# Performance work log

Measured on AMD Instinct MI355X. Metric: run time of the kernel, lower is better.

Reference implementation:

```python
import jax, jax.numpy as jnp
import numpy as np
from jax import lax

BOS, EOS = 1, 2
MAX_LEN = 16
BEAM = 4
VOCAB = 32000
INF = 1e9


def _gather_beams(x, idx):
    # x: [B, K, ...] or [B, K]; idx: [B, k]
    if x.ndim == 3:
        return jnp.take_along_axis(x, idx[:, :, None], axis=1)
    return jnp.take_along_axis(x, idx, axis=1)


def setup_inputs() -> dict:
    key = jax.random.key(0)
    k1, k2, k3, k4 = jax.random.split(key, 4)
    B, S, D = 16, 128, 512
    return {
        "src_input": jax.random.randint(k1, (B, S), 0, VOCAB),
        "E_src": jax.random.normal(k2, (VOCAB, D), jnp.float32) * 0.02,
        "E_tgt": jax.random.normal(k3, (VOCAB, D), jnp.float32) * 0.02,
        "W": jax.random.normal(k4, (D, VOCAB), jnp.float32) * 0.02,
        "b": jnp.zeros((VOCAB,), jnp.float32),
    }


def _beam_search(src_input, E_src, E_tgt, W, b):
    B = src_input.shape[0]
    # tile_by_beam: repeat each batch row beam_size times
    src = jnp.repeat(src_input, BEAM, axis=0)                     # [B*BEAM, S]
    # stub encoder: embedding + masked mean pool (pad token = 0)
    enc = E_src[src]                                              # [B*BEAM, S, D]
    keep = (src != 0).astype(enc.dtype)[..., None]
    pooled = (enc * keep).sum(1) / jnp.maximum(keep.sum(1), 1.0)  # [B*BEAM, D]

    alive_seq = jnp.zeros((B, BEAM, MAX_LEN), jnp.int32).at[:, :, 0].set(BOS)
    alive_lp = jnp.full((B, BEAM), -jnp.inf, jnp.float32).at[:, 0].set(0.0)
    fin_seq = jnp.zeros((B, BEAM, MAX_LEN), jnp.int32)
    fin_scores = jnp.full((B, BEAM), -INF, jnp.float32)
    fin_flags = jnp.zeros((B, BEAM), bool)
    batch_fin = jnp.zeros((B,), bool)
    batch_idx = jnp.arange(B)[:, None]

    for t in range(MAX_LEN - 1):
        # stub decoder: last-token embedding + encoder summary -> vocab logits
        last = alive_seq[:, :, t].reshape(B * BEAM)
        logits = (E_tgt[last] + pooled) @ W + b                   # [B*BEAM, V]
        lp = jax.nn.log_softmax(logits, axis=-1).reshape(B, BEAM, VOCAB)
        log_probs = alive_lp[:, :, None] + lp                     # [B, BEAM, V]
        lpen = jnp.float32(t + 1)
        flat = (log_probs / lpen).reshape(B, BEAM * VOCAB)
        topk_scores, topk_ids = lax.top_k(flat, BEAM * 2)         # [B, 2*BEAM]
        topk_lp = topk_scores * lpen
        if t == 0:
            beam_idx = jnp.tile(jnp.arange(BEAM), (B, 2))
        else:
            beam_idx = topk_ids // VOCAB
        tok = topk_ids % VOCAB
        topk_seq = alive_seq[batch_idx, beam_idx]                 # [B, 2*BEAM, L]
        topk_seq = topk_seq.at[:, :, t + 1].set(tok.astype(jnp.int32))
        topk_fin = tok == EOS
        # alive set: penalize finished candidates
        curr = topk_scores + topk_fin.astype(jnp.float32) * -INF
        _, a_idx = lax.top_k(curr, BEAM)
        alive_seq = _gather_beams(topk_seq, a_idx)
        alive_lp = _gather_beams(topk_lp, a_idx)
        # finished set: penalize unfinished + already-finished batches
        fs = (topk_scores + (1.0 - topk_fin.astype(jnp.float32)) * -INF
              + batch_fin[:, None].astype(jnp.float32) * -INF)
        cand_seq = jnp.concatenate([fin_seq, topk_seq], axis=1)   # [B, 3*BEAM, L]
        cand_sc = jnp.concatenate([fin_scores, fs], axis=1)
        cand_fl = jnp.concatenate([fin_flags, topk_fin], axis=1)
        _, f_idx = lax.top_k(cand_sc, BEAM)
        fin_seq = _gather_beams(cand_seq, f_idx)
        fin_scores = _gather_beams(cand_sc, f_idx)
        fin_flags = _gather_beams(cand_fl, f_idx)
        # batch-finished lower-bound test
        lb_alive = alive_lp[:, 0] / lpen
        lowest_fin = jnp.min(fin_scores * fin_flags.astype(jnp.float32), axis=1)
        lowest_fin = lowest_fin + (1.0 - jnp.all(fin_flags, axis=1).astype(jnp.float32)) * -INF
        batch_fin = batch_fin | (lowest_fin >= lb_alive)
    return fin_seq, fin_scores


def reference(src_input, E_src, E_tgt, W, b):
    fin_seq, _ = _beam_search(src_input, E_src, E_tgt, W, b)
    return fin_seq[:, 0]  # one_best_output [B, MAX_LEN] int32
```

## Files before the change

### kernel.cpp

```cpp
#include <hip/hip_runtime.h>
#include <math.h>

#define BATCH 16
#define SRCLEN 128
#define DIM 512
#define VOCABSZ 32000
#define BEAM 4
#define MAXLEN 16
#define NROWS (BATCH*BEAM)
#define BOS_TOK 1
#define EOS_TOK 2
#define NEGINF 1e9f
#define CHUNKS 8
#define CHUNK 4000
#define PCH 8
#define PCL (SRCLEN/PCH)

__device__ inline unsigned long long packkey(float v, int idx) {
    unsigned int fb = __float_as_uint(v);
    fb = fb ^ ((fb >> 31) ? 0xFFFFFFFFu : 0x80000000u);
    return ((unsigned long long)fb << 32) | (unsigned long long)(0xFFFFFFFFu - (unsigned int)idx);
}
__device__ inline float unpack_val(unsigned long long k) {
    unsigned int fb = (unsigned int)(k >> 32);
    fb = fb ^ ((fb >> 31) ? 0x80000000u : 0xFFFFFFFFu);
    return __uint_as_float(fb);
}
__device__ inline int unpack_id(unsigned long long k) {
    return (int)(0xFFFFFFFFu - (unsigned int)(k & 0xFFFFFFFFu));
}
__device__ inline unsigned long long shflxor64(unsigned long long x, int mask) {
    unsigned int lo = (unsigned int)x, hi = (unsigned int)(x >> 32);
    lo = (unsigned int)__shfl_xor((int)lo, mask, 64);
    hi = (unsigned int)__shfl_xor((int)hi, mask, 64);
    return ((unsigned long long)hi << 32) | (unsigned long long)lo;
}
__device__ inline unsigned long long wavemax64(unsigned long long k) {
#pragma unroll
    for (int off = 1; off < 64; off <<= 1) {
        unsigned long long o = shflxor64(k, off);
        k = (o > k) ? o : k;
    }
    return k;
}

__global__ __launch_bounds__(512) void k_pool2(const int* __restrict__ src,
                                               const float* __restrict__ Esrc,
                                               float* __restrict__ pp, float* __restrict__ pcnt) {
    int b = blockIdx.x, c = blockIdx.y;
    int d = threadIdx.x;
    float acc = 0.f, cnt = 0.f;
#pragma unroll
    for (int s = 0; s < PCL; ++s) {
        int tok = src[b * SRCLEN + c * PCL + s];
        if (tok != 0) { acc += Esrc[(size_t)tok * DIM + d]; cnt += 1.f; }
    }
    pp[(b * PCH + c) * DIM + d] = acc;
    if (d == 0) pcnt[b * PCH + c] = cnt;
}

__global__ __launch_bounds__(512) void k_poolred(const float* __restrict__ pp,
                                                 const float* __restrict__ pcnt,
                                                 float* __restrict__ pooled) {
    int b = blockIdx.x;
    int d = threadIdx.x;
    float acc = 0.f, cnt = 0.f;
#pragma unroll
    for (int c = 0; c < PCH; ++c) { acc += pp[(b * PCH + c) * DIM + d]; cnt += pcnt[b * PCH + c]; }
    pooled[b * DIM + d] = acc / fmaxf(cnt, 1.f);
}

__global__ __launch_bounds__(1024) void k_init(int* __restrict__ alive_seq, float* __restrict__ alive_lp,
                                               int* __restrict__ fin_seq, float* __restrict__ fin_scores,
                                               int* __restrict__ fin_flags, int* __restrict__ batch_fin) {
    int tid = threadIdx.x;
    alive_seq[tid] = (tid % MAXLEN == 0) ? BOS_TOK : 0;
    fin_seq[tid] = 0;
    if (tid < NROWS) {
        alive_lp[tid] = (tid % BEAM == 0) ? 0.f : -INFINITY;
        fin_scores[tid] = -NEGINF;
        fin_flags[tid] = 0;
    }
    if (tid < BATCH) batch_fin[tid] = 0;
}

__global__ __launch_bounds__(512) void k_x(const float* __restrict__ Etgt,
                                           const float* __restrict__ pooled,
                                           const int* __restrict__ alive_seq, int t,
                                           float* __restrict__ xT) {
    int i = blockIdx.x;
    int d = threadIdx.x;
    int last = alive_seq[i * MAXLEN + t];
    float v = Etgt[(size_t)last * DIM + d] + pooled[(i >> 2) * DIM + d];
    xT[d * NROWS + i] = v;
}

template<int GDLEN>
__global__ __launch_bounds__(256) void k_gemm8(const float* __restrict__ xT,
                                               const float* __restrict__ W,
                                               float* __restrict__ partial) {
    int lane = threadIdx.x & 63;
    int r0 = __builtin_amdgcn_readfirstlane((threadIdx.x >> 6) * 16);
    int v0 = blockIdx.x * 256 + lane * 4;
    int z  = blockIdx.z;
    int d0 = z * GDLEN;

    float4 acc[16];
#pragma unroll
    for (int i = 0; i < 16; ++i) acc[i] = make_float4(0.f, 0.f, 0.f, 0.f);

    const float*  wp = W + (size_t)d0 * VOCABSZ + v0;
    const float4* xq = (const float4*)(xT + (size_t)d0 * NROWS + r0);
#pragma unroll 2
    for (int d = 0; d < GDLEN; ++d) {
        float4 wq = *(const float4*)(wp);
        wp += (size_t)VOCABSZ;
        float4 xa = xq[0], xb = xq[1], xc = xq[2], xd = xq[3];
        xq += NROWS / 4;
        float xv[16] = {xa.x, xa.y, xa.z, xa.w, xb.x, xb.y, xb.z, xb.w,
                        xc.x, xc.y, xc.z, xc.w, xd.x, xd.y, xd.z, xd.w};
#pragma unroll
        for (int i = 0; i < 16; ++i) {
            acc[i].x = fmaf(xv[i], wq.x, acc[i].x);
            acc[i].y = fmaf(xv[i], wq.y, acc[i].y);
            acc[i].z = fmaf(xv[i], wq.z, acc[i].z);
            acc[i].w = fmaf(xv[i], wq.w, acc[i].w);
        }
    }

    float* op = partial + (size_t)z * NROWS * VOCABSZ + (size_t)r0 * VOCABSZ + v0;
#pragma unroll
    for (int r = 0; r < 16; ++r)
        *(float4*)(op + (size_t)r * VOCABSZ) = acc[r];
}

template<int NZ>
__global__ __launch_bounds__(1024) void k_part(const float* __restrict__ partial,
                                               const float* __restrict__ bias,
                                               float* __restrict__ pm, float* __restrict__ ps,
                                               float* __restrict__ ptopv, int* __restrict__ ptopi) {
    int row = blockIdx.x, ch = blockIdx.y;
    int tid = threadIdx.x;
    int lane = tid & 63;
    int wv = tid >> 6;
    const size_t slab = (size_t)NROWS * VOCABSZ;
    const bool valid = tid < (CHUNK / 4);

    float vals[4] = {-INFINITY, -INFINITY, -INFINITY, -INFINITY};
    if (valid) {
        const float4* l0 = (const float4*)(partial + (size_t)row * VOCABSZ + ch * CHUNK);
        float4 q = l0[tid];
#pragma unroll
        for (int zz = 1; zz < NZ; ++zz) {
            const float4* lz = (const float4*)(partial + slab * zz + (size_t)row * VOCABSZ + ch * CHUNK);
            float4 q2 = lz[tid];
            q.x += q2.x; q.y += q2.y; q.z += q2.z; q.w += q2.w;
        }
        float4 bb = ((const float4*)(bias + ch * CHUNK))[tid];
        vals[0] = q.x + bb.x; vals[1] = q.y + bb.y; vals[2] = q.z + bb.z; vals[3] = q.w + bb.w;
    }

    float m_t = fmaxf(fmaxf(vals[0], vals[1]), fmaxf(vals[2], vals[3]));
#pragma unroll
    for (int off = 1; off < 64; off <<= 1) m_t = fmaxf(m_t, __shfl_xor(m_t, off, 64));
    __shared__ float swred[16];
    if (lane == 0) swred[wv] = m_t;
    __syncthreads();
    float m = swred[0];
#pragma unroll
    for (int w = 1; w < 16; ++w) m = fmaxf(m, swred[w]);
    __syncthreads();

    float se = 0.f;
    if (valid) {
#pragma unroll
        for (int c = 0; c < 4; ++c) se += expf(vals[c] - m);
    }
#pragma unroll
    for (int off = 1; off < 64; off <<= 1) se += __shfl_xor(se, off, 64);
    if (lane == 0) swred[wv] = se;
    __syncthreads();
    if (tid == 0) {
        float s = 0.f;
#pragma unroll
        for (int w = 0; w < 16; ++w) s += swred[w];
        pm[row * CHUNKS + ch] = m;
        ps[row * CHUNKS + ch] = s;
    }

    int gi = ch * CHUNK + tid * 4;
    unsigned long long k0 = 0ULL, k1 = 0ULL, k2 = 0ULL, k3 = 0ULL;
    if (valid) {
        k0 = packkey(vals[0], gi);
        k1 = packkey(vals[1], gi + 1);
        k2 = packkey(vals[2], gi + 2);
        k3 = packkey(vals[3], gi + 3);
    }
    {
        unsigned long long tswp;
#define CSW(a,b) if (b > a) { tswp = a; a = b; b = tswp; }
        CSW(k0,k1) CSW(k2,k3) CSW(k0,k2) CSW(k1,k3) CSW(k1,k2)
#undef CSW
    }
    __shared__ unsigned long long skey[128];
    {
        int pos = 0;
        unsigned long long wtop[8];
#pragma unroll
        for (int r = 0; r < 8; ++r) {
            unsigned long long head = (pos == 0) ? k0 : (pos == 1) ? k1 :
                                      (pos == 2) ? k2 : (pos == 3) ? k3 : 0ULL;
            unsigned long long mx = wavemax64(head);
            if (head == mx && head != 0ULL) pos++;
            wtop[r] = mx;
        }
        if (lane == 0) {
#pragma unroll
            for (int r = 0; r < 8; ++r) skey[wv * 8 + r] = wtop[r];
        }
    }
    __syncthreads();
    if (tid < 64) {
        unsigned long long a = skey[tid];
        unsigned long long b2 = skey[64 + tid];
        unsigned long long hi = (a > b2) ? a : b2;
        unsigned long long lo = (a > b2) ? b2 : a;
        float* otv = ptopv + ((size_t)row * CHUNKS + ch) * 8;
        int*   oti = ptopi + ((size_t)row * CHUNKS + ch) * 8;
        int pos = 0;
#pragma unroll
        for (int r = 0; r < 8; ++r) {
            unsigned long long head = (pos == 0) ? hi : (pos == 1) ? lo : 0ULL;
            unsigned long long mx = wavemax64(head);
            if (head == mx && head != 0ULL) pos++;
            if (tid == 0) { otv[r] = unpack_val(mx); oti[r] = unpack_id(mx); }
        }
    }
}

__global__ __launch_bounds__(64) void k_mergesel(const float* __restrict__ pm, const float* __restrict__ ps,
                                                 const float* __restrict__ ptopv, const int* __restrict__ ptopi,
                                                 int* __restrict__ alive_seq, float* __restrict__ alive_lp,
                                                 int* __restrict__ fin_seq, float* __restrict__ fin_scores,
                                                 int* __restrict__ fin_flags, int* __restrict__ batch_fin, int t) {
    int b = blockIdx.x;
    int tid = threadIdx.x;
    __shared__ int aseq_old[BEAM][MAXLEN]; __shared__ int fseq_old[BEAM][MAXLEN];
    __shared__ float s_tlp[8]; __shared__ int s_ttok[8], s_tbeam[8];
    __shared__ int s_aidx[4], s_fidx[4];
    __shared__ float s_nfsc[4]; __shared__ int s_nffl[4];
    float lpen = (float)(t + 1);

    { int k = tid >> 4, p = tid & 15;
      aseq_old[k][p] = alive_seq[(b * BEAM + k) * MAXLEN + p];
      fseq_old[k][p] = fin_seq[(b * BEAM + k) * MAXLEN + p]; }

    float rv[4]; int ri[4];
#pragma unroll
    for (int k = 0; k < 4; ++k) {
        rv[k] = ptopv[(size_t)(b * BEAM + k) * 64 + tid];
        ri[k] = ptopi[(size_t)(b * BEAM + k) * 64 + tid];
    }

    float alp[4], fsc[4]; int ffl[4];
#pragma unroll
    for (int k = 0; k < 4; ++k) {
        alp[k] = alive_lp[b * BEAM + k];
        fsc[k] = fin_scores[b * BEAM + k];
        ffl[k] = fin_flags[b * BEAM + k];
    }
    int bf_old = batch_fin[b];

    float srm[4], srl[4];
#pragma unroll
    for (int k = 0; k < 4; ++k) {
        float m = -INFINITY;
#pragma unroll
        for (int c = 0; c < CHUNKS; ++c) m = fmaxf(m, pm[(b * BEAM + k) * CHUNKS + c]);
        float s = 0.f;
#pragma unroll
        for (int c = 0; c < CHUNKS; ++c) s += ps[(b * BEAM + k) * CHUNKS + c] * expf(pm[(b * BEAM + k) * CHUNKS + c] - m);
        srm[k] = m; srl[k] = logf(s);
    }

    unsigned long long key[4];
#pragma unroll
    for (int k = 0; k < 4; ++k) {
        float sh = rv[k] - srm[k];
        float lp = sh - srl[k];
        float full = alp[k] + lp;
        float cv = full / lpen;
        key[k] = packkey(cv, k * VOCABSZ + ri[k]);
    }
    {
        unsigned long long tmp;
#define CSW(a,b) if (key[b] > key[a]) { tmp = key[a]; key[a] = key[b]; key[b] = tmp; }
        CSW(0,1) CSW(2,3) CSW(0,2) CSW(1,3) CSW(1,2)
#undef CSW
    }

    float tscore[8], tlp[8]; int ttok[8], tbeam[8], tfin[8];
    int pos = 0;
#pragma unroll
    for (int r = 0; r < 8; ++r) {
        unsigned long long head = (pos == 0) ? key[0] : (pos == 1) ? key[1] :
                                  (pos == 2) ? key[2] : (pos == 3) ? key[3] : 0ULL;
        unsigned long long mx = wavemax64(head);
        if (head == mx && head != 0ULL) pos++;
        float sc = unpack_val(mx);
        int id = unpack_id(mx);
        tscore[r] = sc;
        tlp[r] = sc * lpen;
        ttok[r] = id % VOCABSZ;
        tbeam[r] = id / VOCABSZ;
        tfin[r] = (ttok[r] == EOS_TOK) ? 1 : 0;
    }

    int aidx[4];
    {
        float curr[8];
#pragma unroll
        for (int j = 0; j < 8; ++j) curr[j] = tscore[j] + (tfin[j] ? -NEGINF : 0.0f);
        unsigned int used = 0;
#pragma unroll
        for (int r = 0; r < 4; ++r) {
            float bv = 0.f; int bj = -1;
#pragma unroll
            for (int j = 0; j < 8; ++j) {
                bool skip = (used >> j) & 1u;
                bool better = !skip && (bj < 0 || curr[j] > bv);
                if (better) { bv = curr[j]; bj = j; }
            }
            used |= 1u << bj; aidx[r] = bj;
        }
    }
    int fidx[4]; float nfsc[4]; int nffl[4];
    {
        float fscand[12]; int fflcand[12];
#pragma unroll
        for (int j = 0; j < 4; ++j) { fscand[j] = fsc[j]; fflcand[j] = ffl[j]; }
#pragma unroll
        for (int q = 0; q < 8; ++q) {
            float t1 = tscore[q] + (tfin[q] ? 0.0f : -NEGINF);
            float t2 = t1 + (bf_old ? -NEGINF : 0.0f);
            fscand[4 + q] = t2; fflcand[4 + q] = tfin[q];
        }
        unsigned int used = 0;
#pragma unroll
        for (int r = 0; r < 4; ++r) {
            float bv = 0.f; int bj = -1;
#pragma unroll
            for (int j = 0; j < 12; ++j) {
                bool skip = (used >> j) & 1u;
                bool better = !skip && (bj < 0 || fscand[j] > bv);
                if (better) { bv = fscand[j]; bj = j; }
            }
            used |= 1u << bj; fidx[r] = bj;
            nfsc[r] = bv;
        }
#pragma unroll
        for (int r = 0; r < 4; ++r) {
            int bj = fidx[r]; int fl = 0;
#pragma unroll
            for (int j = 0; j < 12; ++j) if (bj == j) fl = fflcand[j];
            nffl[r] = fl;
        }
    }

    if (tid == 0) {
#pragma unroll
        for (int r = 0; r < 8; ++r) { s_tlp[r] = tlp[r]; s_ttok[r] = ttok[r]; s_tbeam[r] = tbeam[r]; }
#pragma unroll
        for (int r = 0; r < 4; ++r) { s_aidx[r] = aidx[r]; s_fidx[r] = fidx[r]; s_nfsc[r] = nfsc[r]; s_nffl[r] = nffl[r]; }
    }
    __syncthreads();

    { int k = tid >> 4, p = tid & 15;
      int j = s_aidx[k];
      int val = (p == t + 1) ? s_ttok[j] : aseq_old[s_tbeam[j]][p];
      alive_seq[(b * BEAM + k) * MAXLEN + p] = val;
      int fi = s_fidx[k]; int fval;
      if (fi < 4) fval = fseq_old[fi][p];
      else { int q = fi - 4; fval = (p == t + 1) ? s_ttok[q] : aseq_old[s_tbeam[q]][p]; }
      fin_seq[(b * BEAM + k) * MAXLEN + p] = fval; }

    if (tid < 4) {
        alive_lp[b * BEAM + tid] = s_tlp[s_aidx[tid]];
        fin_scores[b * BEAM + tid] = s_nfsc[tid];
        fin_flags[b * BEAM + tid] = s_nffl[tid];
    }
    if (tid == 0) {
        float lb = s_tlp[s_aidx[0]] / lpen;
        float lowest = nfsc[0] * (nffl[0] ? 1.f : 0.f);
        int allf = nffl[0];
#pragma unroll
        for (int k2 = 1; k2 < 4; ++k2) {
            float pz = nfsc[k2] * (nffl[k2] ? 1.f : 0.f);
            lowest = fminf(lowest, pz);
            allf = allf && nffl[k2];
        }
        lowest = lowest + (allf ? 0.f : -NEGINF);
        batch_fin[b] = bf_old || (lowest >= lb);
    }
}

__global__ __launch_bounds__(256) void k_out(const int* __restrict__ fin_seq, float* __restrict__ out) {
    int tid = threadIdx.x;
    if (tid < BATCH * MAXLEN) {
        int b = tid / MAXLEN, p = tid % MAXLEN;
        out[tid] = (float)fin_seq[(b * BEAM + 0) * MAXLEN + p];
    }
}

extern "C" void kernel_launch(void* const* d_in, const int* in_sizes, int n_in,
                              void* d_out, int out_size, void* d_ws, size_t ws_size,
                              hipStream_t stream) {
    const int*   src  = (const int*)d_in[0];
    const float* Esrc = (const float*)d_in[1];
    const float* Etgt = (const float*)d_in[2];
    const float* W    = (const float*)d_in[3];
    const float* bias = (const float*)d_in[4];
    float* out = (float*)d_out;

    const size_t slab = (size_t)NROWS * VOCABSZ * 4;
    const bool big8 = ws_size >= 8 * slab + (2u << 20);
    const bool big4 = ws_size >= 4 * slab + (2u << 20);
    const int NZ = big8 ? 8 : (big4 ? 4 : 2);

    char* p = (char*)d_ws;
    float* partial    = (float*)p; p += NZ * slab;
    float* pooled     = (float*)p; p += BATCH * DIM * 4;
    float* xT         = (float*)p; p += DIM * NROWS * 4;
    float* pp         = (float*)p; p += BATCH * PCH * DIM * 4;
    float* pcnt       = (float*)p; p += BATCH * PCH * 4;
    float* pm         = (float*)p; p += NROWS * CHUNKS * 4;
    float* ps         = (float*)p; p += NROWS * CHUNKS * 4;
    float* ptopv      = (float*)p; p += NROWS * CHUNKS * 8 * 4;
    int*   ptopi      = (int*)p;   p += NROWS * CHUNKS * 8 * 4;
    int*   alive_seq  = (int*)p;   p += NROWS * MAXLEN * 4;
    int*   fin_seq    = (int*)p;   p += NROWS * MAXLEN * 4;
    float* alive_lp   = (float*)p; p += NROWS * 4;
    float* fin_scores = (float*)p; p += NROWS * 4;
    int*   fin_flags  = (int*)p;   p += NROWS * 4;
    int*   batch_fin  = (int*)p;   p += BATCH * 4;

    k_pool2<<<dim3(BATCH, PCH), DIM, 0, stream>>>(src, Esrc, pp, pcnt);
    k_poolred<<<BATCH, DIM, 0, stream>>>(pp, pcnt, pooled);
    k_init<<<1, 1024, 0, stream>>>(alive_seq, alive_lp, fin_seq, fin_scores, fin_flags, batch_fin);
    for (int t = 0; t < MAXLEN - 1; ++t) {
        k_x<<<NROWS, DIM, 0, stream>>>(Etgt, pooled, alive_seq, t, xT);
        if (big8) {
            k_gemm8<DIM/8><<<dim3(VOCABSZ / 256, 1, 8), 256, 0, stream>>>(xT, W, partial);
            k_part<8><<<dim3(NROWS, CHUNKS), 1024, 0, stream>>>(partial, bias, pm, ps, ptopv, ptopi);
        } else if (big4) {
            k_gemm8<DIM/4><<<dim3(VOCABSZ / 256, 1, 4), 256, 0, stream>>>(xT, W, partial);
            k_part<4><<<dim3(NROWS, CHUNKS), 1024, 0, stream>>>(partial, bias, pm, ps, ptopv, ptopi);
        } else {
            k_gemm8<DIM/2><<<dim3(VOCABSZ / 256, 1, 2), 256, 0, stream>>>(xT, W, partial);
            k_part<2><<<dim3(NROWS, CHUNKS), 1024, 0, stream>>>(partial, bias, pm, ps, ptopv, ptopi);
        }
        k_mergesel<<<BATCH, 64, 0, stream>>>(pm, ps, ptopv, ptopi, alive_seq, alive_lp,
                                             fin_seq, fin_scores, fin_flags, batch_fin, t);
    }
    k_out<<<1, 256, 0, stream>>>(fin_seq, out);
}
```

Baseline: 1.138 ms.

## Stage activations in LDS and software-pipeline W loads in split-K GEMM

The GEMM kernel now copies its slice of the transposed activations into shared memory once per block and reads them from LDS. It also double-buffers the W loads in groups of four rows, so the next group is in flight while the current one is being multiplied. The 8-way split-K path is removed, so the kernel uses 4-way split (or 2-way) with longer K per block and fewer partial slabs for the reduction kernel to read. The trade-offs are fewer blocks in flight, which lowers parallelism, and more registers spent on the prefetched W values.

Measured after the change: 1.078 ms. 5.3% less time.

```diff
diff --git a/kernel.cpp b/kernel.cpp
--- a/kernel.cpp
+++ b/kernel.cpp
@@ -95,8 +95,29 @@
     xT[d * NROWS + i] = v;
 }
 
+#define FMA4(i, xs, wq) \
+    acc[i].x = fmaf((xs),(wq).x,acc[i].x); acc[i].y = fmaf((xs),(wq).y,acc[i].y); \
+    acc[i].z = fmaf((xs),(wq).z,acc[i].z); acc[i].w = fmaf((xs),(wq).w,acc[i].w);
+#define FMAD_LDS(wq, dd) { \
+    float4 xa = *(const float4*)(xsp + (dd) * NROWS);      \
+    float4 xb = *(const float4*)(xsp + (dd) * NROWS + 4);  \
+    float4 xc = *(const float4*)(xsp + (dd) * NROWS + 8);  \
+    float4 xd = *(const float4*)(xsp + (dd) * NROWS + 12); \
+    FMA4(0, xa.x, wq)  FMA4(1, xa.y, wq)  FMA4(2, xa.z, wq)  FMA4(3, xa.w, wq)  \
+    FMA4(4, xb.x, wq)  FMA4(5, xb.y, wq)  FMA4(6, xb.z, wq)  FMA4(7, xb.w, wq)  \
+    FMA4(8, xc.x, wq)  FMA4(9, xc.y, wq)  FMA4(10, xc.z, wq) FMA4(11, xc.w, wq) \
+    FMA4(12, xd.x, wq) FMA4(13, xd.y, wq) FMA4(14, xd.z, wq) FMA4(15, xd.w, wq) }
+#define LOADW(P, dbase) \
+    w##P##0 = *(const float4*)(wp + (size_t)((dbase)+0) * VOCABSZ); \
+    w##P##1 = *(const float4*)(wp + (size_t)((dbase)+1) * VOCABSZ); \
+    w##P##2 = *(const float4*)(wp + (size_t)((dbase)+2) * VOCABSZ); \
+    w##P##3 = *(const float4*)(wp + (size_t)((dbase)+3) * VOCABSZ);
+#define FMACHUNK(P, dbase) \
+    FMAD_LDS(w##P##0, (dbase)+0) FMAD_LDS(w##P##1, (dbase)+1) \
+    FMAD_LDS(w##P##2, (dbase)+2) FMAD_LDS(w##P##3, (dbase)+3)
+
 template<int GDLEN>
-__global__ __launch_bounds__(256) void k_gemm8(const float* __restrict__ xT,
+__global__ __launch_bounds__(256) void k_gemm9(const float* __restrict__ xT,
                                                const float* __restrict__ W,
                                                float* __restrict__ partial) {
     int lane = threadIdx.x & 63;
@@ -105,27 +126,31 @@
     int z  = blockIdx.z;
     int d0 = z * GDLEN;
 
+    __shared__ float xs[GDLEN * NROWS];
+    {
+        const float4* xg = (const float4*)(xT + (size_t)d0 * NROWS);
+        float4* xs4 = (float4*)xs;
+#pragma unroll
+        for (int i = 0; i < (GDLEN * NROWS / 4) / 256; ++i)
+            xs4[i * 256 + threadIdx.x] = xg[i * 256 + threadIdx.x];
+    }
+    __syncthreads();
+
     float4 acc[16];
 #pragma unroll
     for (int i = 0; i < 16; ++i) acc[i] = make_float4(0.f, 0.f, 0.f, 0.f);
 
-    const float*  wp = W + (size_t)d0 * VOCABSZ + v0;
-    const float4* xq = (const float4*)(xT + (size_t)d0 * NROWS + r0);
-#pragma unroll 2
-    for (int d = 0; d < GDLEN; ++d) {
-        float4 wq = *(const float4*)(wp);
-        wp += (size_t)VOCABSZ;
-        float4 xa = xq[0], xb = xq[1], xc = xq[2], xd = xq[3];
-        xq += NROWS / 4;
-        float xv[16] = {xa.x, xa.y, xa.z, xa.w, xb.x, xb.y, xb.z, xb.w,
-                        xc.x, xc.y, xc.z, xc.w, xd.x, xd.y, xd.z, xd.w};
-#pragma unroll
-        for (int i = 0; i < 16; ++i) {
-            acc[i].x = fmaf(xv[i], wq.x, acc[i].x);
-            acc[i].y = fmaf(xv[i], wq.y, acc[i].y);
-            acc[i].z = fmaf(xv[i], wq.z, acc[i].z);
-            acc[i].w = fmaf(xv[i], wq.w, acc[i].w);
-        }
+    const float* wp  = W + (size_t)d0 * VOCABSZ + v0;
+    const float* xsp = xs + r0;
+    float4 wA0, wA1, wA2, wA3, wB0, wB1, wB2, wB3;
+
+    const int nc = GDLEN / 4;
+    LOADW(A, 0)
+    for (int c = 0; c < nc; c += 2) {
+        LOADW(B, (c + 1) * 4)
+        FMACHUNK(A, c * 4)
+        if (c + 2 < nc) { LOADW(A, (c + 2) * 4) }
+        FMACHUNK(B, (c + 1) * 4)
     }
 
     float* op = partial + (size_t)z * NROWS * VOCABSZ + (size_t)r0 * VOCABSZ + v0;
@@ -423,9 +448,8 @@
     float* out = (float*)d_out;
 
     const size_t slab = (size_t)NROWS * VOCABSZ * 4;
-    const bool big8 = ws_size >= 8 * slab + (2u << 20);
     const bool big4 = ws_size >= 4 * slab + (2u << 20);
-    const int NZ = big8 ? 8 : (big4 ? 4 : 2);
+    const int NZ = big4 ? 4 : 2;
 
     char* p = (char*)d_ws;
     float* partial    = (float*)p; p += NZ * slab;
@@ -449,14 +473,11 @@
     k_init<<<1, 1024, 0, stream>>>(alive_seq, alive_lp, fin_seq, fin_scores, fin_flags, batch_fin);
     for (int t = 0; t < MAXLEN - 1; ++t) {
         k_x<<<NROWS, DIM, 0, stream>>>(Etgt, pooled, alive_seq, t, xT);
-        if (big8) {
-            k_gemm8<DIM/8><<<dim3(VOCABSZ / 256, 1, 8), 256, 0, stream>>>(xT, W, partial);
-            k_part<8><<<dim3(NROWS, CHUNKS), 1024, 0, stream>>>(partial, bias, pm, ps, ptopv, ptopi);
-        } else if (big4) {
-            k_gemm8<DIM/4><<<dim3(VOCABSZ / 256, 1, 4), 256, 0, stream>>>(xT, W, partial);
+        if (big4) {
+            k_gemm9<DIM/4><<<dim3(VOCABSZ / 256, 1, 4), 256, 0, stream>>>(xT, W, partial);
             k_part<4><<<dim3(NROWS, CHUNKS), 1024, 0, stream>>>(partial, bias, pm, ps, ptopv, ptopi);
         } else {
-            k_gemm8<DIM/2><<<dim3(VOCABSZ / 256, 1, 2), 256, 0, stream>>>(xT, W, partial);
+            k_gemm9<DIM/2><<<dim3(VOCABSZ / 256, 1, 2), 256, 0, stream>>>(xT, W, partial);
             k_part<2><<<dim3(NROWS, CHUNKS), 1024, 0, stream>>>(partial, bias, pm, ps, ptopv, ptopi);
         }
         k_mergesel<<<BATCH, 64, 0, stream>>>(pm, ps, ptopv, ptopi, alive_seq, alive_lp,
```
